# Kernel tuning notes

Hardware: AMD Instinct MI355X
Metric: run time of the kernel (lower is better)

## Reference

```python
import jax, jax.numpy as jnp
import numpy as np

N_NODES = 30000
N_EDGES = 480000
F_IN = 64
F_EDGE = 16
HID = 128
N_LAYERS = 3
N_CLASSES = 10
MSG_EPS = 1e-7   # GENConv eps added after ReLU
SM_EPS = 1e-16   # PyG softmax denom eps
LN_EPS = 1e-5


def _layer_norm(x, g, b):
    m = jnp.mean(x, axis=-1, keepdims=True)
    v = jnp.mean((x - m) ** 2, axis=-1, keepdims=True)
    return (x - m) * jax.lax.rsqrt(v + LN_EPS) * g + b


def _gen_conv(h, ea, src, dst, t, w1, b1, lg, lb, w2, b2):
    # GENConv message: relu(x_j + e_ij) + eps  -> [E, H]
    msg = jax.nn.relu(h[src] + ea) + MSG_EPS
    # learnable-temperature segment softmax over incoming edges of each node
    logits = msg * t
    mx = jax.ops.segment_max(logits, dst, num_segments=N_NODES)
    e = jnp.exp(logits - mx[dst])
    s = jax.ops.segment_sum(e, dst, num_segments=N_NODES)
    alpha = e / (s[dst] + SM_EPS)
    agg = jax.ops.segment_sum(msg * alpha, dst, num_segments=N_NODES)  # [N, H]
    # out = MLP(aggr + x): Linear(H,2H) -> LayerNorm -> ReLU -> Linear(2H,H)
    z = agg + h
    z = jax.nn.relu(_layer_norm(z @ w1 + b1, lg, lb)) @ w2 + b2
    return z


def setup_inputs() -> dict:
    key = jax.random.key(0)
    ks = jax.random.split(key, 10)
    g = lambda k, s, sc=0.05: jax.random.normal(k, s, jnp.float32) * sc
    return {
        "x": g(ks[0], (N_NODES, F_IN), 1.0),
        "edge_attr": g(ks[1], (N_EDGES, F_EDGE), 1.0),
        "node_enc_w": g(ks[2], (F_IN, HID)),
        "node_enc_b": jnp.zeros((HID,), jnp.float32),
        "edge_enc_w": g(ks[3], (F_EDGE, HID)),
        "edge_enc_b": jnp.zeros((HID,), jnp.float32),
        "mlp1_w": g(ks[4], (N_LAYERS, HID, 2 * HID)),
        "mlp1_b": jnp.zeros((N_LAYERS, 2 * HID), jnp.float32),
        "mlp_ln_g": jnp.ones((N_LAYERS, 2 * HID), jnp.float32),
        "mlp_ln_b": jnp.zeros((N_LAYERS, 2 * HID), jnp.float32),
        "mlp2_w": g(ks[5], (N_LAYERS, 2 * HID, HID)),
        "mlp2_b": jnp.zeros((N_LAYERS, HID), jnp.float32),
        "t": jnp.ones((N_LAYERS,), jnp.float32),
        "norm_g": jnp.ones((N_LAYERS, HID), jnp.float32),
        "norm_b": jnp.zeros((N_LAYERS, HID), jnp.float32),
        "lin_w": g(ks[6], (HID, N_CLASSES)),
        "lin_b": jnp.zeros((N_CLASSES,), jnp.float32),
        "edge_index": jax.random.randint(ks[7], (2, N_EDGES), 0, N_NODES, jnp.int32),
    }


def reference(x, edge_attr, node_enc_w, node_enc_b, edge_enc_w, edge_enc_b,
              mlp1_w, mlp1_b, mlp_ln_g, mlp_ln_b, mlp2_w, mlp2_b, t,
              norm_g, norm_b, lin_w, lin_b, edge_index):
    src, dst = edge_index[0], edge_index[1]
    ea = edge_attr @ edge_enc_w + edge_enc_b   # [E, H]
    h = x @ node_enc_w + node_enc_b            # [N, H]
    # first layer applies the conv directly (as in the original forward)
    h = _gen_conv(h, ea, src, dst, t[0], mlp1_w[0], mlp1_b[0],
                  mlp_ln_g[0], mlp_ln_b[0], mlp2_w[0], mlp2_b[0])
    # remaining DeepGCN res+ layers: h = h + conv(dropout(relu(norm(h))))
    for i in range(1, N_LAYERS):
        res = h
        z = jax.nn.relu(_layer_norm(h, norm_g[i], norm_b[i]))  # dropout p=0.1 -> identity in eval
        z = _gen_conv(z, ea, src, dst, t[i], mlp1_w[i], mlp1_b[i],
                      mlp_ln_g[i], mlp_ln_b[i], mlp2_w[i], mlp2_b[i])
        h = z + res
    # final norm/act from layers[0] then classifier (dropout -> identity in eval)
    h = jax.nn.relu(_layer_norm(h, norm_g[0], norm_b[0]))
    return h @ lin_w + lin_b
```

## Files before the change

kernel.cpp:

```cpp
#include <hip/hip_runtime.h>
#include <hip/hip_bf16.h>

#define NN 30000
#define NE 480000
#define NROWT 1875

typedef __attribute__((ext_vector_type(8))) short short8;
typedef __attribute__((ext_vector_type(4))) float floatx4;

__device__ __forceinline__ short f2bs(float f) {
    __hip_bfloat16 h = __float2bfloat16(f);
    return *reinterpret_cast<short*>(&h);
}

__device__ __forceinline__ short2 split_bf16(float f) {
    __hip_bfloat16 h = __float2bfloat16(f);
    float r = f - __bfloat162float(h);
    __hip_bfloat16 l = __float2bfloat16(r);
    short2 out;
    out.x = *reinterpret_cast<short*>(&h);
    out.y = *reinterpret_cast<short*>(&l);
    return out;
}

__global__ void presplit_all(const float* __restrict__ ew, const float* __restrict__ nw,
                             const float* __restrict__ m1w, const float* __restrict__ m2w,
                             const float* __restrict__ lw,
                             short* __restrict__ ew_h, short* __restrict__ ew_l,
                             short* __restrict__ nw_h, short* __restrict__ nw_l,
                             short* __restrict__ m1_h, short* __restrict__ m1_l,
                             short* __restrict__ m2_h, short* __restrict__ m2_l,
                             short* __restrict__ lw_h, short* __restrict__ lw_l)
{
    int i = blockIdx.x * 256 + threadIdx.x;
    if (i < 2048) {
        int k = i >> 7, n = i & 127;
        short2 s = split_bf16(ew[i]);
        ew_h[n * 16 + k] = s.x; ew_l[n * 16 + k] = s.y;
    } else if (i < 10240) {
        int j = i - 2048;
        int k = j >> 7, n = j & 127;
        short2 s = split_bf16(nw[j]);
        nw_h[n * 64 + k] = s.x; nw_l[n * 64 + k] = s.y;
    } else if (i < 108544) {
        int j = i - 10240;
        int l = j >> 15, jj = j & 32767;
        int k = jj >> 8, n = jj & 255;
        short2 s = split_bf16(m1w[j]);
        m1_h[(size_t)l * 32768 + n * 128 + k] = s.x;
        m1_l[(size_t)l * 32768 + n * 128 + k] = s.y;
    } else if (i < 206848) {
        int j = i - 108544;
        int l = j >> 15, jj = j & 32767;
        int k = jj >> 7, n = jj & 127;
        short2 s = split_bf16(m2w[j]);
        m2_h[(size_t)l * 32768 + n * 256 + k] = s.x;
        m2_l[(size_t)l * 32768 + n * 256 + k] = s.y;
    } else if (i < 208896) {
        int j = i - 206848;
        int k = j >> 4, n = j & 15;
        short2 s = (n < 10) ? split_bf16(lw[k * 10 + n]) : short2{0, 0};
        lw_h[n * 128 + k] = s.x; lw_l[n * 128 + k] = s.y;
    }
}

template<int K, int N>
__launch_bounds__(256)
__global__ void gemm_a32(const float* __restrict__ A, const short* __restrict__ Bh,
                         const short* __restrict__ Bl, const float* __restrict__ bias,
                         float* __restrict__ C, int total_waves)
{
    int wave = ((blockIdx.x * 256) + threadIdx.x) >> 6;
    if (wave >= total_waves) return;
    constexpr int NT = N / 16;
    const int mt = wave / NT, nt = wave % NT;
    const int lane = threadIdx.x & 63;
    const int l15 = lane & 15, quad = lane >> 4;
    const int row = mt * 16 + l15;
    const int col = nt * 16 + l15;
    floatx4 acc = {0.f, 0.f, 0.f, 0.f};
#pragma unroll
    for (int k0 = 0; k0 < K; k0 += 32) {
        const int kb = k0 + quad * 8;
        short8 ah, al;
        const float* ap = A + (size_t)row * K + kb;
        floatx4 a0 = *(const floatx4*)ap;
        floatx4 a1 = *(const floatx4*)(ap + 4);
#pragma unroll
        for (int j = 0; j < 4; j++) {
            short2 s0 = split_bf16(a0[j]); ah[j] = s0.x; al[j] = s0.y;
            short2 s1 = split_bf16(a1[j]); ah[j + 4] = s1.x; al[j + 4] = s1.y;
        }
        short8 bh = *(const short8*)(Bh + (size_t)col * K + kb);
        short8 bl = *(const short8*)(Bl + (size_t)col * K + kb);
        acc = __builtin_amdgcn_mfma_f32_16x16x32_bf16(ah, bh, acc, 0, 0, 0);
        acc = __builtin_amdgcn_mfma_f32_16x16x32_bf16(al, bh, acc, 0, 0, 0);
        acc = __builtin_amdgcn_mfma_f32_16x16x32_bf16(ah, bl, acc, 0, 0, 0);
    }
    float bv = bias[col];
#pragma unroll
    for (int r = 0; r < 4; r++) {
        int ro = mt * 16 + quad * 4 + r;
        C[(size_t)ro * N + col] = acc[r] + bv;
    }
}

template<int K, int NTOT, int NTW, int NREAL>
__launch_bounds__(256)
__global__ void gemm_s(const short* __restrict__ Ah, const short* __restrict__ Al,
                       const short* __restrict__ Bh, const short* __restrict__ Bl,
                       const float* __restrict__ bias, float* __restrict__ C, int total_waves)
{
    int wave = ((blockIdx.x * 256) + threadIdx.x) >> 6;
    if (wave >= total_waves) return;
    constexpr int NG = NTOT / (16 * NTW);
    const int mt = wave / NG, g = wave % NG;
    const int lane = threadIdx.x & 63;
    const int l15 = lane & 15, quad = lane >> 4;
    const int row = mt * 16 + l15;
    floatx4 acc[NTW];
#pragma unroll
    for (int t = 0; t < NTW; t++) acc[t] = {0.f, 0.f, 0.f, 0.f};
#pragma unroll
    for (int k0 = 0; k0 < K; k0 += 32) {
        const int kb = k0 + quad * 8;
        short8 ah = *(const short8*)(Ah + (size_t)row * K + kb);
        short8 al = *(const short8*)(Al + (size_t)row * K + kb);
#pragma unroll
        for (int t = 0; t < NTW; t++) {
            int col = g * NTW * 16 + t * 16 + l15;
            short8 bh = *(const short8*)(Bh + (size_t)col * K + kb);
            short8 bl = *(const short8*)(Bl + (size_t)col * K + kb);
            acc[t] = __builtin_amdgcn_mfma_f32_16x16x32_bf16(ah, bh, acc[t], 0, 0, 0);
            acc[t] = __builtin_amdgcn_mfma_f32_16x16x32_bf16(al, bh, acc[t], 0, 0, 0);
            acc[t] = __builtin_amdgcn_mfma_f32_16x16x32_bf16(ah, bl, acc[t], 0, 0, 0);
        }
    }
#pragma unroll
    for (int t = 0; t < NTW; t++) {
        int col = g * NTW * 16 + t * 16 + l15;
        if (col < NREAL) {
            float bv = bias[col];
#pragma unroll
            for (int r = 0; r < 4; r++) {
                int ro = mt * 16 + quad * 4 + r;
                C[(size_t)ro * NREAL + col] = acc[t][r] + bv;
            }
        }
    }
}

__launch_bounds__(256)
__global__ void gemm_ea(const float* __restrict__ edge_attr, const int* __restrict__ eidx_csr,
                        const short* __restrict__ Bh, const short* __restrict__ Bl,
                        const float* __restrict__ bias, unsigned* __restrict__ ea4)
{
    __shared__ short tile[2][16][132];
    const int wv = threadIdx.x >> 6;
    const int sub = wv >> 1, g = wv & 1;
    const int lane = threadIdx.x & 63;
    const int l15 = lane & 15, quad = lane >> 4;
    const int p = blockIdx.x * 32 + sub * 16 + l15;
    short8 a;
    if (quad < 2) {
        int e = eidx_csr[p];
        const float* ap = edge_attr + (size_t)e * 16 + quad * 8;
        floatx4 a0 = *(const floatx4*)ap;
        floatx4 a1 = *(const floatx4*)(ap + 4);
#pragma unroll
        for (int j = 0; j < 4; j++) { a[j] = f2bs(a0[j]); a[j + 4] = f2bs(a1[j]); }
    } else {
#pragma unroll
        for (int j = 0; j < 8; j++) a[j] = 0;
    }
    floatx4 acc[4];
#pragma unroll
    for (int t = 0; t < 4; t++) acc[t] = {0.f, 0.f, 0.f, 0.f};
#pragma unroll
    for (int t = 0; t < 4; t++) {
        int col = g * 64 + t * 16 + l15;
        short8 bh, bl;
        if (quad < 2) {
            bh = *(const short8*)(Bh + (size_t)col * 16 + quad * 8);
            bl = *(const short8*)(Bl + (size_t)col * 16 + quad * 8);
        } else {
#pragma unroll
            for (int j = 0; j < 8; j++) { bh[j] = 0; bl[j] = 0; }
        }
        acc[t] = __builtin_amdgcn_mfma_f32_16x16x32_bf16(a, bh, acc[t], 0, 0, 0);
        acc[t] = __builtin_amdgcn_mfma_f32_16x16x32_bf16(a, bl, acc[t], 0, 0, 0);
    }
#pragma unroll
    for (int t = 0; t < 4; t++) {
        int col = g * 64 + t * 16 + l15;
        float bv = bias[col];
#pragma unroll
        for (int r = 0; r < 4; r++)
            tile[sub][quad * 4 + r][col] = f2bs(acc[t][r] + bv);
    }
    __syncthreads();
#pragma unroll
    for (int c = 0; c < 2; c++) {
        int idx = threadIdx.x + 256 * c;
        int o = idx * 16;
        int g4l = o >> 10;
        int lp = (o & 1023) >> 4;
        unsigned u[4];
#pragma unroll
        for (int e = 0; e < 4; e++) {
            int rl = g4l * 4 + e;
            u[e] = *(const unsigned*)&tile[rl >> 4][rl & 15][2 * lp];
        }
        uint4 val = make_uint4(u[0], u[1], u[2], u[3]);
        *(uint4*)((char*)ea4 + (size_t)blockIdx.x * 8192 + o) = val;
    }
}

__global__ void zero_kernel(int* __restrict__ p, int n)
{
    int i = blockIdx.x * 256 + threadIdx.x;
    if (i < n) p[i] = 0;
}

__global__ void hist_kernel(const int* __restrict__ dst, int* __restrict__ count)
{
    int e = blockIdx.x * 256 + threadIdx.x;
    if (e < NE) atomicAdd(count + dst[e], 1);
}

__launch_bounds__(1024)
__global__ void scan_kernel(const int* __restrict__ count, int* __restrict__ rowptr)
{
    __shared__ int part[1024];
    const int t = threadIdx.x;
    const int CH = (NN + 1023) / 1024;
    const int base = t * CH;
    int sum = 0;
    for (int j = 0; j < CH; j++) {
        int idx = base + j;
        if (idx < NN) sum += count[idx];
    }
    part[t] = sum;
    __syncthreads();
    for (int d = 1; d < 1024; d <<= 1) {
        int v = (t >= d) ? part[t - d] : 0;
        __syncthreads();
        part[t] += v;
        __syncthreads();
    }
    int off = (t == 0) ? 0 : part[t - 1];
    for (int j = 0; j < CH; j++) {
        int idx = base + j;
        if (idx < NN) { rowptr[idx] = off; off += count[idx]; }
    }
    if (t == 1023) rowptr[NN] = part[1023];
}

__global__ void scatter_kernel(const int* __restrict__ src, const int* __restrict__ dst,
                               const int* __restrict__ rowptr, int* __restrict__ cursor,
                               int* __restrict__ src_csr, int* __restrict__ eidx_csr)
{
    int e = blockIdx.x * 256 + threadIdx.x;
    if (e >= NE) return;
    int d = dst[e];
    int pos = rowptr[d] + atomicAdd(cursor + d, 1);
    src_csr[pos] = src[e];
    eidx_csr[pos] = e;
}

__device__ __forceinline__ void upd(float hv, float av, float tt, float& s, float& n)
{
    float g = fmaxf(hv + av, 0.f) + 1e-7f;
    float e = __expf(g * tt);
    s += e;
    n = fmaf(g, e, n);
}

__launch_bounds__(256)
__global__ void agg_kernel(const float* __restrict__ hin, const uint4* __restrict__ ea4q,
                           const unsigned* __restrict__ ea4u, const int* __restrict__ src_csr,
                           const int* __restrict__ rowptr, const float* __restrict__ tptr,
                           int layer, short* __restrict__ Zh, short* __restrict__ Zl)
{
    int node = (blockIdx.x * 256 + threadIdx.x) >> 6;
    if (node >= NN) return;
    const int lane = threadIdx.x & 63;
    const float tt = tptr[layer];
    const float2* h2 = (const float2*)hin;
    int j = rowptr[node];
    const int end = rowptr[node + 1];
    float s0 = 0.f, s1 = 0.f, n0 = 0.f, n1 = 0.f;
    while (j < end && (j & 3)) {
        unsigned u = ea4u[(((size_t)(j >> 2)) << 8) + lane * 4 + (j & 3)];
        float2 ha = h2[(size_t)src_csr[j] * 64 + lane];
        upd(ha.x, __uint_as_float(u << 16), tt, s0, n0);
        upd(ha.y, __uint_as_float(u & 0xffff0000u), tt, s1, n1);
        j++;
    }
    for (; j + 4 <= end; j += 4) {
        uint4 uu = ea4q[(((size_t)(j >> 2)) << 6) + lane];
        int4 sv = *(const int4*)(src_csr + j);
        float2 ha = h2[(size_t)sv.x * 64 + lane];
        float2 hb = h2[(size_t)sv.y * 64 + lane];
        float2 hc = h2[(size_t)sv.z * 64 + lane];
        float2 hd = h2[(size_t)sv.w * 64 + lane];
        upd(ha.x, __uint_as_float(uu.x << 16), tt, s0, n0);
        upd(ha.y, __uint_as_float(uu.x & 0xffff0000u), tt, s1, n1);
        upd(hb.x, __uint_as_float(uu.y << 16), tt, s0, n0);
        upd(hb.y, __uint_as_float(uu.y & 0xffff0000u), tt, s1, n1);
        upd(hc.x, __uint_as_float(uu.z << 16), tt, s0, n0);
        upd(hc.y, __uint_as_float(uu.z & 0xffff0000u), tt, s1, n1);
        upd(hd.x, __uint_as_float(uu.w << 16), tt, s0, n0);
        upd(hd.y, __uint_as_float(uu.w & 0xffff0000u), tt, s1, n1);
    }
    for (; j < end; j++) {
        unsigned u = ea4u[(((size_t)(j >> 2)) << 8) + lane * 4 + (j & 3)];
        float2 ha = h2[(size_t)src_csr[j] * 64 + lane];
        upd(ha.x, __uint_as_float(u << 16), tt, s0, n0);
        upd(ha.y, __uint_as_float(u & 0xffff0000u), tt, s1, n1);
    }
    float2 res = h2[(size_t)node * 64 + lane];
    float ox = n0 / (s0 + 1e-16f) + res.x;
    float oy = n1 / (s1 + 1e-16f) + res.y;
    short2 sx = split_bf16(ox), sy = split_bf16(oy);
    ((unsigned*)Zh)[(size_t)node * 64 + lane] =
        (unsigned)(unsigned short)sx.x | ((unsigned)(unsigned short)sy.x << 16);
    ((unsigned*)Zl)[(size_t)node * 64 + lane] =
        (unsigned)(unsigned short)sx.y | ((unsigned)(unsigned short)sy.y << 16);
}

template<bool HAS_RES, bool FINAL>
__launch_bounds__(256)
__global__ void mlp_fused(const short* __restrict__ Ah, const short* __restrict__ Al,
                          const short* __restrict__ B1h, const short* __restrict__ B1l,
                          const float* __restrict__ b1, const float* __restrict__ g1,
                          const float* __restrict__ be1,
                          const short* __restrict__ B2h, const short* __restrict__ B2l,
                          const float* __restrict__ b2, const float* __restrict__ res,
                          const float* __restrict__ g2, const float* __restrict__ be2,
                          short* __restrict__ z1h, short* __restrict__ z1l,
                          float* __restrict__ Hout, float* __restrict__ HinOut,
                          short* __restrict__ Fh, short* __restrict__ Fl)
{
    __shared__ __align__(16) short lds[32768];
    const int wv = threadIdx.x >> 6;
    const int lane = threadIdx.x & 63;
    const int l15 = lane & 15, quad = lane >> 4;
    const int tile = blockIdx.x * 4 + wv;
    const bool valid = (tile < NROWT);
    const int row = tile * 16 + l15;

    floatx4 acc[16];
#pragma unroll
    for (int t = 0; t < 16; t++) acc[t] = {0.f, 0.f, 0.f, 0.f};
    for (int hf = 0; hf < 2; hf++) {
        __syncthreads();
        {
            const float4* s1p = (const float4*)(B1h + hf * 16384);
            const float4* s2p = (const float4*)(B1l + hf * 16384);
            float4* d = (float4*)lds;
#pragma unroll
            for (int i = 0; i < 8; i++) {
                int t8 = threadIdx.x + 256 * i;
                int col = t8 >> 4, k8 = t8 & 15;
                int unit = col * 16 + (k8 ^ (col & 15));
                d[unit] = s1p[t8];
                d[2048 + unit] = s2p[t8];
            }
        }
        __syncthreads();
        if (valid) {
#pragma unroll
            for (int k0 = 0; k0 < 128; k0 += 32) {
                const int kb = k0 + quad * 8;
                const int kb8 = kb >> 3;
                short8 ah = *(const short8*)(Ah + (size_t)row * 128 + kb);
                short8 al = *(const short8*)(Al + (size_t)row * 128 + kb);
#pragma unroll
                for (int t = 0; t < 8; t++) {
                    int col = t * 16 + l15;
                    int unit = col * 16 + (kb8 ^ (col & 15));
                    const short* bp = lds + unit * 8;
                    short8 bh = *(const short8*)bp;
                    short8 bl = *(const short8*)(bp + 16384);
                    int ti = hf * 8 + t;
                    acc[ti] = __builtin_amdgcn_mfma_f32_16x16x32_bf16(ah, bh, acc[ti], 0, 0, 0);
                    acc[ti] = __builtin_amdgcn_mfma_f32_16x16x32_bf16(al, bh, acc[ti], 0, 0, 0);
                    acc[ti] = __builtin_amdgcn_mfma_f32_16x16x32_bf16(ah, bl, acc[ti], 0, 0, 0);
                }
            }
        }
    }
    if (valid) {
#pragma unroll
        for (int t = 0; t < 16; t++) {
            float bv = b1[t * 16 + l15];
#pragma unroll
            for (int r = 0; r < 4; r++) acc[t][r] += bv;
        }
        float s1[4] = {0.f, 0.f, 0.f, 0.f}, s2[4] = {0.f, 0.f, 0.f, 0.f};
#pragma unroll
        for (int t = 0; t < 16; t++)
#pragma unroll
            for (int r = 0; r < 4; r++) { s1[r] += acc[t][r]; s2[r] += acc[t][r] * acc[t][r]; }
#pragma unroll
        for (int m = 1; m <= 8; m <<= 1)
#pragma unroll
            for (int r = 0; r < 4; r++) {
                s1[r] += __shfl_xor(s1[r], m, 64);
                s2[r] += __shfl_xor(s2[r], m, 64);
            }
        float mean[4], rstd[4];
#pragma unroll
        for (int r = 0; r < 4; r++) {
            mean[r] = s1[r] * (1.f / 256.f);
            float var = s2[r] * (1.f / 256.f) - mean[r] * mean[r];
            rstd[r] = rsqrtf(var + 1e-5f);
        }
#pragma unroll
        for (int t = 0; t < 16; t++) {
            int col = t * 16 + l15;
            float gg = g1[col], bb = be1[col];
#pragma unroll
            for (int r = 0; r < 4; r++) {
                float y = fmaxf((acc[t][r] - mean[r]) * rstd[r] * gg + bb, 0.f);
                short2 sp = split_bf16(y);
                int ro = tile * 16 + quad * 4 + r;
                z1h[(size_t)ro * 256 + col] = sp.x;
                z1l[(size_t)ro * 256 + col] = sp.y;
            }
        }
    }
    floatx4 acc2[8];
#pragma unroll
    for (int t = 0; t < 8; t++) acc2[t] = {0.f, 0.f, 0.f, 0.f};
    for (int hf = 0; hf < 2; hf++) {
        __syncthreads();
        {
            const float4* s1p = (const float4*)(B2h + hf * 16384);
            const float4* s2p = (const float4*)(B2l + hf * 16384);
            float4* d = (float4*)lds;
#pragma unroll
            for (int i = 0; i < 8; i++) {
                int t8 = threadIdx.x + 256 * i;
                int col = t8 >> 5, k8 = t8 & 31;
                int unit = col * 32 + (k8 ^ (col & 15));
                d[unit] = s1p[t8];
                d[2048 + unit] = s2p[t8];
            }
        }
        __syncthreads();
        if (valid) {
#pragma unroll
            for (int k0 = 0; k0 < 256; k0 += 32) {
                const int kb = k0 + quad * 8;
                const int kb8 = kb >> 3;
                short8 zh = *(const short8*)(z1h + (size_t)row * 256 + kb);
                short8 zl = *(const short8*)(z1l + (size_t)row * 256 + kb);
#pragma unroll
                for (int t = 0; t < 4; t++) {
                    int col = t * 16 + l15;
                    int unit = col * 32 + (kb8 ^ (col & 15));
                    const short* bp = lds + unit * 8;
                    short8 bh = *(const short8*)bp;
                    short8 bl = *(const short8*)(bp + 16384);
                    int ti = hf * 4 + t;
                    acc2[ti] = __builtin_amdgcn_mfma_f32_16x16x32_bf16(zh, bh, acc2[ti], 0, 0, 0);
                    acc2[ti] = __builtin_amdgcn_mfma_f32_16x16x32_bf16(zl, bh, acc2[ti], 0, 0, 0);
                    acc2[ti] = __builtin_amdgcn_mfma_f32_16x16x32_bf16(zh, bl, acc2[ti], 0, 0, 0);
                }
            }
        }
    }
    if (valid) {
#pragma unroll
        for (int t = 0; t < 8; t++) {
            int col = t * 16 + l15;
            float bv = b2[col];
#pragma unroll
            for (int r = 0; r < 4; r++) {
                acc2[t][r] += bv;
                if (HAS_RES) {
                    int ro = tile * 16 + quad * 4 + r;
                    acc2[t][r] += res[(size_t)ro * 128 + col];
                }
            }
        }
        float s1[4] = {0.f, 0.f, 0.f, 0.f}, s2[4] = {0.f, 0.f, 0.f, 0.f};
#pragma unroll
        for (int t = 0; t < 8; t++)
#pragma unroll
            for (int r = 0; r < 4; r++) { s1[r] += acc2[t][r]; s2[r] += acc2[t][r] * acc2[t][r]; }
#pragma unroll
        for (int m = 1; m <= 8; m <<= 1)
#pragma unroll
            for (int r = 0; r < 4; r++) {
                s1[r] += __shfl_xor(s1[r], m, 64);
                s2[r] += __shfl_xor(s2[r], m, 64);
            }
        float mean[4], rstd[4];
#pragma unroll
        for (int r = 0; r < 4; r++) {
            mean[r] = s1[r] * (1.f / 128.f);
            float var = s2[r] * (1.f / 128.f) - mean[r] * mean[r];
            rstd[r] = rsqrtf(var + 1e-5f);
        }
#pragma unroll
        for (int t = 0; t < 8; t++) {
            int col = t * 16 + l15;
            float gg = g2[col], bb = be2[col];
#pragma unroll
            for (int r = 0; r < 4; r++) {
                int ro = tile * 16 + quad * 4 + r;
                float x = acc2[t][r];
                float y = fmaxf((x - mean[r]) * rstd[r] * gg + bb, 0.f);
                if (FINAL) {
                    short2 sp = split_bf16(y);
                    Fh[(size_t)ro * 128 + col] = sp.x;
                    Fl[(size_t)ro * 128 + col] = sp.y;
                } else {
                    Hout[(size_t)ro * 128 + col] = x;
                    HinOut[(size_t)ro * 128 + col] = y;
                }
            }
        }
    }
}

extern "C" void kernel_launch(void* const* d_in, const int* in_sizes, int n_in,
                              void* d_out, int out_size, void* d_ws, size_t ws_size,
                              hipStream_t stream)
{
    const float* x         = (const float*)d_in[0];
    const float* edge_attr = (const float*)d_in[1];
    const float* nw        = (const float*)d_in[2];
    const float* nb        = (const float*)d_in[3];
    const float* ew        = (const float*)d_in[4];
    const float* eb        = (const float*)d_in[5];
    const float* m1w       = (const float*)d_in[6];
    const float* m1b       = (const float*)d_in[7];
    const float* lng       = (const float*)d_in[8];
    const float* lnb       = (const float*)d_in[9];
    const float* m2w       = (const float*)d_in[10];
    const float* m2b       = (const float*)d_in[11];
    const float* tpr       = (const float*)d_in[12];
    const float* ng        = (const float*)d_in[13];
    const float* nbb       = (const float*)d_in[14];
    const float* lw        = (const float*)d_in[15];
    const float* lb        = (const float*)d_in[16];
    const int* ei  = (const int*)d_in[17];
    const int* src = ei;
    const int* dst = ei + NE;

    char* w = (char*)d_ws;
    unsigned* ea4 = (unsigned*)w; w += (size_t)NE * 128 * 2;
    int* src_csr  = (int*)w; w += (size_t)NE * 4;
    int* eidx_csr = (int*)w; w += (size_t)NE * 4;
    float* h   = (float*)w; w += (size_t)NN * 128 * 4;
    float* hin = (float*)w; w += (size_t)NN * 128 * 4;
    short* zbuf_h = (short*)w; w += (size_t)NN * 128 * 2;
    short* zbuf_l = (short*)w; w += (size_t)NN * 128 * 2;
    short* fin_h  = (short*)w; w += (size_t)NN * 128 * 2;
    short* fin_l  = (short*)w; w += (size_t)NN * 128 * 2;
    short* z1s_h  = (short*)w; w += (size_t)NN * 256 * 2;
    short* z1s_l  = (short*)w; w += (size_t)NN * 256 * 2;
    short* ew_h = (short*)w; w += (size_t)128 * 16 * 2;
    short* ew_l = (short*)w; w += (size_t)128 * 16 * 2;
    short* nw_h = (short*)w; w += (size_t)128 * 64 * 2;
    short* nw_l = (short*)w; w += (size_t)128 * 64 * 2;
    short* m1_h = (short*)w; w += (size_t)3 * 256 * 128 * 2;
    short* m1_l = (short*)w; w += (size_t)3 * 256 * 128 * 2;
    short* m2_h = (short*)w; w += (size_t)3 * 128 * 256 * 2;
    short* m2_l = (short*)w; w += (size_t)3 * 128 * 256 * 2;
    short* lw_h = (short*)w; w += (size_t)16 * 128 * 2;
    short* lw_l = (short*)w; w += (size_t)16 * 128 * 2;
    int* count  = (int*)w;   w += (size_t)NN * 4;
    int* cursor = (int*)w;   w += (size_t)NN * 4;
    int* rowptr = (int*)w;   w += (size_t)(NN + 1) * 4;

    zero_kernel<<<(2 * NN + 255) / 256, 256, 0, stream>>>(count, 2 * NN);
    hist_kernel<<<(NE + 255) / 256, 256, 0, stream>>>(dst, count);
    scan_kernel<<<1, 1024, 0, stream>>>(count, rowptr);
    scatter_kernel<<<(NE + 255) / 256, 256, 0, stream>>>(src, dst, rowptr, cursor,
                                                         src_csr, eidx_csr);

    presplit_all<<<(208896 + 255) / 256, 256, 0, stream>>>(
        ew, nw, m1w, m2w, lw, ew_h, ew_l, nw_h, nw_l, m1_h, m1_l, m2_h, m2_l, lw_h, lw_l);

    gemm_ea<<<NE / 32, 256, 0, stream>>>(edge_attr, eidx_csr, ew_h, ew_l, eb, ea4);
    gemm_a32<64, 128><<<(NN / 16) * 8 / 4, 256, 0, stream>>>(x, nw_h, nw_l, nb, h, (NN / 16) * 8);

    const uint4* ea4q = (const uint4*)ea4;
    const int mgrid = (NROWT + 3) / 4;
    for (int layer = 0; layer < 3; ++layer) {
        const float* hi = (layer == 0) ? h : hin;
        agg_kernel<<<NN / 4, 256, 0, stream>>>(hi, ea4q, ea4, src_csr, rowptr, tpr, layer,
                                               zbuf_h, zbuf_l);
        if (layer == 0) {
            mlp_fused<false, false><<<mgrid, 256, 0, stream>>>(
                zbuf_h, zbuf_l, m1_h, m1_l, m1b, lng, lnb,
                m2_h, m2_l, m2b, nullptr, ng + 128, nbb + 128,
                z1s_h, z1s_l, h, hin, nullptr, nullptr);
        } else if (layer == 1) {
            mlp_fused<true, false><<<mgrid, 256, 0, stream>>>(
                zbuf_h, zbuf_l, m1_h + 32768, m1_l + 32768, m1b + 256, lng + 256, lnb + 256,
                m2_h + 32768, m2_l + 32768, m2b + 128, h, ng + 256, nbb + 256,
                z1s_h, z1s_l, h, hin, nullptr, nullptr);
        } else {
            mlp_fused<true, true><<<mgrid, 256, 0, stream>>>(
                zbuf_h, zbuf_l, m1_h + 65536, m1_l + 65536, m1b + 512, lng + 512, lnb + 512,
                m2_h + 65536, m2_l + 65536, m2b + 256, h, ng, nbb,
                z1s_h, z1s_l, nullptr, nullptr, fin_h, fin_l);
        }
    }
    gemm_s<128, 16, 1, 10><<<((NN / 16) + 3) / 4, 256, 0, stream>>>(
        fin_h, fin_l, lw_h, lw_l, lb, (float*)d_out, NN / 16);
}
```

Measured before the change: 536.8 us.

## Gather bf16-packed node features in aggregation and unroll edge groups with masks

The producing GEMM and MLP kernels now also write a bf16-packed copy of the node features, and the aggregation kernel gathers those 4-byte values per lane instead of float2. This halves the bytes of the random source-node gathers, which are the main memory cost of the aggregation. The aggregation loop also processes aligned groups of four edges with validity masks, two groups at a time into separate accumulators, which removes the scalar head and tail loops and adds some wasted work on partial groups. It lowers the precision of the gathered messages to bf16, which risks accuracy against the fp32 reference.

```diff
diff --git a/kernel.cpp b/kernel.cpp
--- a/kernel.cpp
+++ b/kernel.cpp
@@ -68,7 +68,7 @@
 __launch_bounds__(256)
 __global__ void gemm_a32(const float* __restrict__ A, const short* __restrict__ Bh,
                          const short* __restrict__ Bl, const float* __restrict__ bias,
-                         float* __restrict__ C, int total_waves)
+                         float* __restrict__ C, unsigned* __restrict__ hp, int total_waves)
 {
     int wave = ((blockIdx.x * 256) + threadIdx.x) >> 6;
     if (wave >= total_waves) return;
@@ -101,7 +101,12 @@
 #pragma unroll
     for (int r = 0; r < 4; r++) {
         int ro = mt * 16 + quad * 4 + r;
-        C[(size_t)ro * N + col] = acc[r] + bv;
+        float v = acc[r] + bv;
+        C[(size_t)ro * N + col] = v;
+        int mb = (int)(unsigned short)f2bs(v);
+        int ob = __shfl_xor(mb, 1, 64);
+        if ((l15 & 1) == 0)
+            hp[(size_t)ro * 64 + nt * 8 + (l15 >> 1)] = (unsigned)mb | ((unsigned)ob << 16);
     }
 }
 
@@ -268,17 +273,18 @@
     eidx_csr[pos] = e;
 }
 
-__device__ __forceinline__ void upd(float hv, float av, float tt, float& s, float& n)
+__device__ __forceinline__ void updm(float hv, float av, float tt, float m,
+                                     float& s, float& n)
 {
     float g = fmaxf(hv + av, 0.f) + 1e-7f;
-    float e = __expf(g * tt);
+    float e = __expf(g * tt) * m;
     s += e;
     n = fmaf(g, e, n);
 }
 
 __launch_bounds__(256)
-__global__ void agg_kernel(const float* __restrict__ hin, const uint4* __restrict__ ea4q,
-                           const unsigned* __restrict__ ea4u, const int* __restrict__ src_csr,
+__global__ void agg_kernel(const unsigned* __restrict__ hp, const float* __restrict__ hres,
+                           const uint4* __restrict__ ea4q, const int* __restrict__ src_csr,
                            const int* __restrict__ rowptr, const float* __restrict__ tptr,
                            int layer, short* __restrict__ Zh, short* __restrict__ Zl)
 {
@@ -286,40 +292,45 @@
     if (node >= NN) return;
     const int lane = threadIdx.x & 63;
     const float tt = tptr[layer];
-    const float2* h2 = (const float2*)hin;
-    int j = rowptr[node];
+    const int start = rowptr[node];
     const int end = rowptr[node + 1];
+    const int g0 = start >> 2, g1 = (end + 3) >> 2;
     float s0 = 0.f, s1 = 0.f, n0 = 0.f, n1 = 0.f;
-    while (j < end && (j & 3)) {
-        unsigned u = ea4u[(((size_t)(j >> 2)) << 8) + lane * 4 + (j & 3)];
-        float2 ha = h2[(size_t)src_csr[j] * 64 + lane];
-        upd(ha.x, __uint_as_float(u << 16), tt, s0, n0);
-        upd(ha.y, __uint_as_float(u & 0xffff0000u), tt, s1, n1);
-        j++;
-    }
-    for (; j + 4 <= end; j += 4) {
-        uint4 uu = ea4q[(((size_t)(j >> 2)) << 6) + lane];
-        int4 sv = *(const int4*)(src_csr + j);
-        float2 ha = h2[(size_t)sv.x * 64 + lane];
-        float2 hb = h2[(size_t)sv.y * 64 + lane];
-        float2 hc = h2[(size_t)sv.z * 64 + lane];
-        float2 hd = h2[(size_t)sv.w * 64 + lane];
-        upd(ha.x, __uint_as_float(uu.x << 16), tt, s0, n0);
-        upd(ha.y, __uint_as_float(uu.x & 0xffff0000u), tt, s1, n1);
-        upd(hb.x, __uint_as_float(uu.y << 16), tt, s0, n0);
-        upd(hb.y, __uint_as_float(uu.y & 0xffff0000u), tt, s1, n1);
-        upd(hc.x, __uint_as_float(uu.z << 16), tt, s0, n0);
-        upd(hc.y, __uint_as_float(uu.z & 0xffff0000u), tt, s1, n1);
-        upd(hd.x, __uint_as_float(uu.w << 16), tt, s0, n0);
-        upd(hd.y, __uint_as_float(uu.w & 0xffff0000u), tt, s1, n1);
-    }
-    for (; j < end; j++) {
-        unsigned u = ea4u[(((size_t)(j >> 2)) << 8) + lane * 4 + (j & 3)];
-        float2 ha = h2[(size_t)src_csr[j] * 64 + lane];
-        upd(ha.x, __uint_as_float(u << 16), tt, s0, n0);
-        upd(ha.y, __uint_as_float(u & 0xffff0000u), tt, s1, n1);
-    }
-    float2 res = h2[(size_t)node * 64 + lane];
+    float s0b = 0.f, s1b = 0.f, n0b = 0.f, n1b = 0.f;
+
+#define PROC(GG, S0, S1, N0, N1)                                                   \
+    {                                                                              \
+        uint4 uu = ea4q[((size_t)(GG) << 6) + lane];                               \
+        int4 sv = *(const int4*)(src_csr + 4 * (GG));                              \
+        int jb = 4 * (GG);                                                         \
+        float m0 = (jb     >= start && jb     < end) ? 1.f : 0.f;                  \
+        float m1 = (jb + 1 >= start && jb + 1 < end) ? 1.f : 0.f;                  \
+        float m2 = (jb + 2 >= start && jb + 2 < end) ? 1.f : 0.f;                  \
+        float m3 = (jb + 3 >= start && jb + 3 < end) ? 1.f : 0.f;                  \
+        unsigned ha = hp[(size_t)sv.x * 64 + lane];                                \
+        unsigned hb = hp[(size_t)sv.y * 64 + lane];                                \
+        unsigned hc = hp[(size_t)sv.z * 64 + lane];                                \
+        unsigned hd = hp[(size_t)sv.w * 64 + lane];                                \
+        updm(__uint_as_float(ha << 16), __uint_as_float(uu.x << 16), tt, m0, S0, N0); \
+        updm(__uint_as_float(ha & 0xffff0000u), __uint_as_float(uu.x & 0xffff0000u), tt, m0, S1, N1); \
+        updm(__uint_as_float(hb << 16), __uint_as_float(uu.y << 16), tt, m1, S0, N0); \
+        updm(__uint_as_float(hb & 0xffff0000u), __uint_as_float(uu.y & 0xffff0000u), tt, m1, S1, N1); \
+        updm(__uint_as_float(hc << 16), __uint_as_float(uu.z << 16), tt, m2, S0, N0); \
+        updm(__uint_as_float(hc & 0xffff0000u), __uint_as_float(uu.z & 0xffff0000u), tt, m2, S1, N1); \
+        updm(__uint_as_float(hd << 16), __uint_as_float(uu.w << 16), tt, m3, S0, N0); \
+        updm(__uint_as_float(hd & 0xffff0000u), __uint_as_float(uu.w & 0xffff0000u), tt, m3, S1, N1); \
+    }
+
+    int g = g0;
+    for (; g + 2 <= g1; g += 2) {
+        PROC(g, s0, s1, n0, n1);
+        PROC(g + 1, s0b, s1b, n0b, n1b);
+    }
+    if (g < g1) PROC(g, s0, s1, n0, n1);
+#undef PROC
+    s0 += s0b; s1 += s1b; n0 += n0b; n1 += n1b;
+
+    float2 res = ((const float2*)hres)[(size_t)node * 64 + lane];
     float ox = n0 / (s0 + 1e-16f) + res.x;
     float oy = n1 / (s1 + 1e-16f) + res.y;
     short2 sx = split_bf16(ox), sy = split_bf16(oy);
@@ -340,6 +351,7 @@
                           const float* __restrict__ g2, const float* __restrict__ be2,
                           short* __restrict__ z1h, short* __restrict__ z1l,
                           float* __restrict__ Hout, float* __restrict__ HinOut,
+                          unsigned* __restrict__ HP,
                           short* __restrict__ Fh, short* __restrict__ Fl)
 {
     __shared__ __align__(16) short lds[32768];
@@ -521,6 +533,11 @@
                 } else {
                     Hout[(size_t)ro * 128 + col] = x;
                     HinOut[(size_t)ro * 128 + col] = y;
+                    int yb = (int)(unsigned short)f2bs(y);
+                    int ob = __shfl_xor(yb, 1, 64);
+                    if ((l15 & 1) == 0)
+                        HP[(size_t)ro * 64 + t * 8 + (l15 >> 1)] =
+                            (unsigned)yb | ((unsigned)ob << 16);
                 }
             }
         }
@@ -556,6 +573,7 @@
     unsigned* ea4 = (unsigned*)w; w += (size_t)NE * 128 * 2;
     int* src_csr  = (int*)w; w += (size_t)NE * 4;
     int* eidx_csr = (int*)w; w += (size_t)NE * 4;
+    unsigned* hp  = (unsigned*)w; w += (size_t)NN * 64 * 4;
     float* h   = (float*)w; w += (size_t)NN * 128 * 4;
     float* hin = (float*)w; w += (size_t)NN * 128 * 4;
     short* zbuf_h = (short*)w; w += (size_t)NN * 128 * 2;
@@ -588,29 +606,30 @@
         ew, nw, m1w, m2w, lw, ew_h, ew_l, nw_h, nw_l, m1_h, m1_l, m2_h, m2_l, lw_h, lw_l);
 
     gemm_ea<<<NE / 32, 256, 0, stream>>>(edge_attr, eidx_csr, ew_h, ew_l, eb, ea4);
-    gemm_a32<64, 128><<<(NN / 16) * 8 / 4, 256, 0, stream>>>(x, nw_h, nw_l, nb, h, (NN / 16) * 8);
+    gemm_a32<64, 128><<<(NN / 16) * 8 / 4, 256, 0, stream>>>(x, nw_h, nw_l, nb, h, hp,
+                                                             (NN / 16) * 8);
 
     const uint4* ea4q = (const uint4*)ea4;
     const int mgrid = (NROWT + 3) / 4;
     for (int layer = 0; layer < 3; ++layer) {
         const float* hi = (layer == 0) ? h : hin;
-        agg_kernel<<<NN / 4, 256, 0, stream>>>(hi, ea4q, ea4, src_csr, rowptr, tpr, layer,
+        agg_kernel<<<NN / 4, 256, 0, stream>>>(hp, hi, ea4q, src_csr, rowptr, tpr, layer,
                                                zbuf_h, zbuf_l);
         if (layer == 0) {
             mlp_fused<false, false><<<mgrid, 256, 0, stream>>>(
                 zbuf_h, zbuf_l, m1_h, m1_l, m1b, lng, lnb,
                 m2_h, m2_l, m2b, nullptr, ng + 128, nbb + 128,
-                z1s_h, z1s_l, h, hin, nullptr, nullptr);
+                z1s_h, z1s_l, h, hin, hp, nullptr, nullptr);
         } else if (layer == 1) {
             mlp_fused<true, false><<<mgrid, 256, 0, stream>>>(
                 zbuf_h, zbuf_l, m1_h + 32768, m1_l + 32768, m1b + 256, lng + 256, lnb + 256,
                 m2_h + 32768, m2_l + 32768, m2b + 128, h, ng + 256, nbb + 256,
-                z1s_h, z1s_l, h, hin, nullptr, nullptr);
+                z1s_h, z1s_l, h, hin, hp, nullptr, nullptr);
         } else {
             mlp_fused<true, true><<<mgrid, 256, 0, stream>>>(
                 zbuf_h, zbuf_l, m1_h + 65536, m1_l + 65536, m1b + 512, lng + 512, lnb + 512,
                 m2_h + 65536, m2_l + 65536, m2b + 256, h, ng, nbb,
-                z1s_h, z1s_l, nullptr, nullptr, fin_h, fin_l);
+                z1s_h, z1s_l, nullptr, nullptr, nullptr, fin_h, fin_l);
         }
     }
     gemm_s<128, 16, 1, 10><<<((NN / 16) + 3) / 4, 256, 0, stream>>>(
```

After: 507.9 us. -5.4%, faster.
